# Optimization experiments

Measured on AMD Instinct MI355X. Metric: run time of the kernel, lower is better.

Reference implementation:

```python
import jax, jax.numpy as jnp
import numpy as np

N = 50000      # nodes
E = 800000     # edges
IN, HID, OUT, H = 128, 32, 128, 4
NEG_SLOPE = 0.2  # DGL GATConv default


def setup_inputs() -> dict:
    key = jax.random.key(0)
    ks = jax.random.split(key, 12)
    def w(k, shape, fan_in):
        return jax.random.normal(k, shape, dtype=jnp.float32) / np.sqrt(fan_in)
    return {
        "x": jax.random.normal(ks[0], (N, IN), dtype=jnp.float32),
        "src": jax.random.randint(ks[1], (E,), 0, N, dtype=jnp.int64),
        "dst": jax.random.randint(ks[2], (E,), 0, N, dtype=jnp.int64),
        # layer 0: GATConv(IN -> HID, H heads)
        "W0": w(ks[3], (IN, H * HID), IN),
        "attn_l0": w(ks[4], (H, HID), HID),
        "attn_r0": w(ks[5], (H, HID), HID),
        "bias0": jnp.zeros((H * HID,), dtype=jnp.float32),
        # layer 1: GATConv(H*HID -> OUT, 1 head)
        "W1": w(ks[6], (H * HID, OUT), H * HID),
        "attn_l1": w(ks[7], (1, OUT), OUT),
        "attn_r1": w(ks[8], (1, OUT), OUT),
        "bias1": jnp.zeros((OUT,), dtype=jnp.float32),
    }


def gat_conv(x, src, dst, W, attn_l, attn_r, bias, heads, feat_dim):
    """DGL GATConv: linear -> per-edge LeakyReLU attention -> edge softmax over
    destination neighborhoods -> weighted scatter-sum -> bias -> ELU."""
    n = x.shape[0]
    feat = (x @ W).reshape(n, heads, feat_dim)            # [N,H,F]
    el = jnp.einsum("nhf,hf->nh", feat, attn_l)           # [N,H]
    er = jnp.einsum("nhf,hf->nh", feat, attn_r)
    e = jax.nn.leaky_relu(el[src] + er[dst], NEG_SLOPE)    # [E,H]
    # segment softmax over incoming edges of each destination node
    e_max = jax.ops.segment_max(e, dst, num_segments=n)    # [N,H]
    exp_e = jnp.exp(e - e_max[dst])                        # [E,H]
    denom = jax.ops.segment_sum(exp_e, dst, num_segments=n)
    alpha = exp_e / denom[dst]                             # [E,H]
    msg = feat[src] * alpha[:, :, None]                    # [E,H,F]
    rst = jax.ops.segment_sum(msg, dst, num_segments=n)    # [N,H,F]
    rst = rst + bias.reshape(heads, feat_dim)
    return jax.nn.elu(rst)


def reference(x, src, dst, W0, attn_l0, attn_r0, bias0, W1, attn_l1, attn_r1, bias1):
    h = gat_conv(x, src, dst, W0, attn_l0, attn_r0, bias0, H, HID)   # [N,H,HID]
    h = h.reshape(h.shape[0], H * HID)                               # flatten(1)
    h = gat_conv(h, src, dst, W1, attn_l1, attn_r1, bias1, 1, OUT)   # [N,1,OUT]
    return h.mean(axis=1)                                            # [N,OUT]
```

## Files before the change

kernel.cpp:

```cpp
#include <hip/hip_runtime.h>

#define NEG_SLOPE 0.2f
#define NBMAX 256
#define BCAP 8192

typedef __attribute__((ext_vector_type(8))) short bf16x8;
typedef __attribute__((ext_vector_type(16))) float f32x16;

__device__ inline ushort bf16rne(float f) {
  uint u = __float_as_uint(f);
  u += 0x7fff + ((u >> 16) & 1);
  return (ushort)(u >> 16);
}
__device__ inline float bf2f(ushort h) { return __uint_as_float((uint)h << 16); }

#define XS(row, byte) ((byte) ^ (((row) & 15) << 4))

__global__ __launch_bounds__(256) void splitW2(const float* __restrict__ W0,
    const float* __restrict__ W1, ushort* __restrict__ W0h, ushort* __restrict__ W0l,
    ushort* __restrict__ W1h, ushort* __restrict__ W1l, int* __restrict__ bucketCursor) {
  if (blockIdx.x == 0 && threadIdx.x < NBMAX) bucketCursor[threadIdx.x] = 0;
  int g = blockIdx.x * 256 + threadIdx.x;
  const float* W = (g < 16384) ? W0 : W1;
  ushort* Wh = (g < 16384) ? W0h : W1h;
  ushort* Wl = (g < 16384) ? W0l : W1l;
  int i = g & 16383;
  int k = i >> 7, nn = i & 127;
  float w = W[i];
  ushort h = bf16rne(w);
  float lo = w - bf2f(h);
  Wh[nn * 128 + k] = h;
  Wl[nn * 128 + k] = bf16rne(lo);
}

__global__ __launch_bounds__(256) void prep_attn(const float* __restrict__ W0,
    const float* __restrict__ W1, const float* __restrict__ al0,
    const float* __restrict__ ar0, const float* __restrict__ al1,
    const float* __restrict__ ar1, float* __restrict__ wl0, float* __restrict__ wr0,
    float* __restrict__ wl1, float* __restrict__ wr1) {
  const int t = threadIdx.x;
  if (t < 128) {
    const int k = t;
#pragma unroll
    for (int h = 0; h < 4; ++h) {
      float sl = 0.f, sr = 0.f;
#pragma unroll
      for (int f = 0; f < 32; ++f) {
        float w = W0[k * 128 + h * 32 + f];
        sl += w * al0[h * 32 + f];
        sr += w * ar0[h * 32 + f];
      }
      wl0[h * 128 + k] = sl;
      wr0[h * 128 + k] = sr;
    }
  } else {
    const int k = t - 128;
    float sl = 0.f, sr = 0.f;
#pragma unroll
    for (int f = 0; f < 128; ++f) {
      float w = W1[k * 128 + f];
      sl += w * al1[f];
      sr += w * ar1[f];
    }
    wl1[k] = sl;
    wr1[k] = sr;
  }
}

__global__ __launch_bounds__(256) void gemm_mfma(const float* __restrict__ A,
    const ushort* __restrict__ Wh, const ushort* __restrict__ Wl,
    ushort* __restrict__ Cb, int n) {
  __shared__ __align__(16) ushort sAh[64 * 128];
  __shared__ __align__(16) ushort sAl[64 * 128];
  const int t = threadIdx.x;
  const int row0 = blockIdx.x * 64;
  const int col0 = blockIdx.y * 64;
  for (int i = t; i < 2048; i += 256) {
    int r = i >> 5, c4 = i & 31;
    int gr = row0 + r;
    float4 v = make_float4(0.f, 0.f, 0.f, 0.f);
    if (gr < n) v = ((const float4*)(A + (size_t)gr * 128))[c4];
    ushort4 h, l;
    h.x = bf16rne(v.x); l.x = bf16rne(v.x - bf2f(h.x));
    h.y = bf16rne(v.y); l.y = bf16rne(v.y - bf2f(h.y));
    h.z = bf16rne(v.z); l.z = bf16rne(v.z - bf2f(h.z));
    h.w = bf16rne(v.w); l.w = bf16rne(v.w - bf2f(h.w));
    int byte = XS(r, r * 256 + c4 * 8);
    *(ushort4*)((char*)sAh + byte) = h;
    *(ushort4*)((char*)sAl + byte) = l;
  }
  __syncthreads();
  const int wv = t >> 6, lane = t & 63;
  const int rbase = (wv >> 1) * 32;
  const int cbase = (wv & 1) * 32;
  const int lr = lane & 31;
  const int hi = lane >> 5;
  const int arow = rbase + lr;
  const int gcol = col0 + cbase + lr;
  const ushort* WhRow = Wh + (size_t)gcol * 128;
  const ushort* WlRow = Wl + (size_t)gcol * 128;
  f32x16 acc0 = {};
  f32x16 acc1 = {};
#pragma unroll
  for (int ks = 0; ks < 8; ++ks) {
    int k16 = ks * 16 + hi * 8;
    int kb = k16 * 2;
    bf16x8 ah = *(bf16x8*)((char*)sAh + XS(arow, arow * 256 + kb));
    bf16x8 al = *(bf16x8*)((char*)sAl + XS(arow, arow * 256 + kb));
    bf16x8 bh = *(const bf16x8*)(WhRow + k16);
    bf16x8 bl = *(const bf16x8*)(WlRow + k16);
    if (ks & 1) {
      acc1 = __builtin_amdgcn_mfma_f32_32x32x16_bf16(ah, bh, acc1, 0, 0, 0);
      acc1 = __builtin_amdgcn_mfma_f32_32x32x16_bf16(ah, bl, acc1, 0, 0, 0);
      acc1 = __builtin_amdgcn_mfma_f32_32x32x16_bf16(al, bh, acc1, 0, 0, 0);
    } else {
      acc0 = __builtin_amdgcn_mfma_f32_32x32x16_bf16(ah, bh, acc0, 0, 0, 0);
      acc0 = __builtin_amdgcn_mfma_f32_32x32x16_bf16(ah, bl, acc0, 0, 0, 0);
      acc0 = __builtin_amdgcn_mfma_f32_32x32x16_bf16(al, bh, acc0, 0, 0, 0);
    }
  }
#pragma unroll
  for (int r = 0; r < 16; ++r) {
    int grow = row0 + rbase + (r & 3) + 8 * (r >> 2) + 4 * hi;
    if (grow < n) Cb[(size_t)grow * 128 + gcol] = bf16rne(acc0[r] + acc1[r]);
  }
}

template <int HEADS>
__global__ __launch_bounds__(256) void node_attn(const float* __restrict__ A,
    const float* __restrict__ wl, const float* __restrict__ wr,
    float* __restrict__ el, float* __restrict__ er, int n) {
  __shared__ float swl[HEADS * 128];
  __shared__ float swr[HEADS * 128];
  for (int i = threadIdx.x; i < HEADS * 128; i += 256) {
    swl[i] = wl[i];
    swr[i] = wr[i];
  }
  __syncthreads();
  int i = blockIdx.x * 256 + threadIdx.x;
  if (i >= n) return;
  const float4* a4 = (const float4*)(A + (size_t)i * 128);
  float accl[HEADS], accr[HEADS];
#pragma unroll
  for (int h = 0; h < HEADS; ++h) { accl[h] = 0.f; accr[h] = 0.f; }
#pragma unroll 8
  for (int k4 = 0; k4 < 32; ++k4) {
    float4 v = a4[k4];
#pragma unroll
    for (int h = 0; h < HEADS; ++h) {
      float4 a = ((const float4*)(swl + h * 128))[k4];
      float4 b = ((const float4*)(swr + h * 128))[k4];
      accl[h] += v.x * a.x + v.y * a.y + v.z * a.z + v.w * a.w;
      accr[h] += v.x * b.x + v.y * b.y + v.z * b.z + v.w * b.w;
    }
  }
  if (HEADS == 4) {
    *(float4*)(el + (size_t)i * 4) = make_float4(accl[0], accl[1], accl[2], accl[3]);
    *(float4*)(er + (size_t)i * 4) = make_float4(accr[0], accr[1], accr[2], accr[3]);
  } else {
    el[i] = accl[0];
    er[i] = accr[0];
  }
}

__global__ __launch_bounds__(1024) void bucket_scatter(const int* __restrict__ src,
    const int* __restrict__ dst, int* __restrict__ bucketCursor,
    uint* __restrict__ bucketData, int E_) {
  __shared__ int h[NBMAX];
  __shared__ int bse[NBMAX];
  const int t = threadIdx.x;
  if (t < NBMAX) h[t] = 0;
  __syncthreads();
  const int base = blockIdx.x * 4096;
  int sv[4], dv[4], bk[4];
  bool ok[4];
#pragma unroll
  for (int k = 0; k < 4; ++k) {
    int i = base + k * 1024 + t;
    ok[k] = i < E_;
    if (ok[k]) {
      sv[k] = src[i];
      dv[k] = dst[i];
      bk[k] = dv[k] >> 8;
      atomicAdd(&h[bk[k]], 1);
    }
  }
  __syncthreads();
  if (t < NBMAX) {
    int c = h[t];
    bse[t] = c ? atomicAdd(&bucketCursor[t], c) : 0;
    h[t] = 0;
  }
  __syncthreads();
#pragma unroll
  for (int k = 0; k < 4; ++k) {
    if (ok[k]) {
      int r = atomicAdd(&h[bk[k]], 1);
      int pos = bse[bk[k]] + r;
      if (pos < BCAP)
        bucketData[(size_t)bk[k] * BCAP + pos] = (uint)sv[k] | ((uint)(dv[k] & 255) << 16);
    }
  }
}

__global__ __launch_bounds__(1024) void fine_csr(const uint* __restrict__ bucketData,
    const int* __restrict__ bucketCursor, int* __restrict__ rowbeg,
    int* __restrict__ rowend, uint* __restrict__ csr, int n) {
  __shared__ int fh[256];
  __shared__ int fx[256];
  const int b = blockIdx.x;
  const int t = threadIdx.x;
  const int beg = b * BCAP;
  int cnt = bucketCursor[b];
  if (cnt > BCAP) cnt = BCAP;
  if (t < 256) fh[t] = 0;
  __syncthreads();
  for (int i = t; i < cnt; i += 1024) atomicAdd(&fh[bucketData[beg + i] >> 16], 1);
  __syncthreads();
  if (t < 256) fx[t] = fh[t];
  __syncthreads();
  for (int off = 1; off < 256; off <<= 1) {
    int u = 0;
    if (t < 256 && t >= off) u = fx[t - off];
    __syncthreads();
    if (t < 256) fx[t] += u;
    __syncthreads();
  }
  if (t < 256) {
    int excl = fx[t] - fh[t];
    int node = b * 256 + t;
    if (node < n) {
      rowbeg[node] = beg + excl;
      rowend[node] = beg + fx[t];
    }
    fh[t] = excl;
  }
  __syncthreads();
  for (int i = t; i < cnt; i += 1024) {
    uint rec = bucketData[beg + i];
    int r = atomicAdd(&fh[rec >> 16], 1);
    csr[beg + r] = rec;
  }
}

__global__ __launch_bounds__(256) void aggregate4(const int* __restrict__ rowbeg,
    const int* __restrict__ rowend, const uint* __restrict__ csr,
    const ushort* __restrict__ featb, const float* __restrict__ el,
    const float* __restrict__ er, const float* __restrict__ bias,
    float* __restrict__ out, int n) {
  int node = blockIdx.x * 4 + (threadIdx.x >> 6);
  if (node >= n) return;
  const int lane = threadIdx.x & 63;
  const int f0 = lane * 2;
  const int h = lane >> 4;
  const float erh = er[(size_t)node * 4 + h];
  float a0 = 0.f, a1 = 0.f, d = 0.f;
  const int beg = rowbeg[node], end = rowend[node];
  int idx = beg;
  for (; idx + 7 < end; idx += 8) {
    int s0 = csr[idx + 0] & 0xffffu;
    int s1 = csr[idx + 1] & 0xffffu;
    int s2 = csr[idx + 2] & 0xffffu;
    int s3 = csr[idx + 3] & 0xffffu;
    int s4 = csr[idx + 4] & 0xffffu;
    int s5 = csr[idx + 5] & 0xffffu;
    int s6 = csr[idx + 6] & 0xffffu;
    int s7 = csr[idx + 7] & 0xffffu;
    float l0 = el[(size_t)s0 * 4 + h];
    float l1 = el[(size_t)s1 * 4 + h];
    float l2 = el[(size_t)s2 * 4 + h];
    float l3 = el[(size_t)s3 * 4 + h];
    float l4 = el[(size_t)s4 * 4 + h];
    float l5 = el[(size_t)s5 * 4 + h];
    float l6 = el[(size_t)s6 * 4 + h];
    float l7 = el[(size_t)s7 * 4 + h];
    uint v0 = *(const uint*)(featb + (size_t)s0 * 128 + f0);
    uint v1 = *(const uint*)(featb + (size_t)s1 * 128 + f0);
    uint v2 = *(const uint*)(featb + (size_t)s2 * 128 + f0);
    uint v3 = *(const uint*)(featb + (size_t)s3 * 128 + f0);
    uint v4 = *(const uint*)(featb + (size_t)s4 * 128 + f0);
    uint v5 = *(const uint*)(featb + (size_t)s5 * 128 + f0);
    uint v6 = *(const uint*)(featb + (size_t)s6 * 128 + f0);
    uint v7 = *(const uint*)(featb + (size_t)s7 * 128 + f0);
    float e0 = l0 + erh; e0 = e0 > 0.f ? e0 : NEG_SLOPE * e0; float w0 = __expf(e0);
    float e1 = l1 + erh; e1 = e1 > 0.f ? e1 : NEG_SLOPE * e1; float w1 = __expf(e1);
    float e2 = l2 + erh; e2 = e2 > 0.f ? e2 : NEG_SLOPE * e2; float w2 = __expf(e2);
    float e3 = l3 + erh; e3 = e3 > 0.f ? e3 : NEG_SLOPE * e3; float w3 = __expf(e3);
    float e4 = l4 + erh; e4 = e4 > 0.f ? e4 : NEG_SLOPE * e4; float w4 = __expf(e4);
    float e5 = l5 + erh; e5 = e5 > 0.f ? e5 : NEG_SLOPE * e5; float w5 = __expf(e5);
    float e6 = l6 + erh; e6 = e6 > 0.f ? e6 : NEG_SLOPE * e6; float w6 = __expf(e6);
    float e7 = l7 + erh; e7 = e7 > 0.f ? e7 : NEG_SLOPE * e7; float w7 = __expf(e7);
    a0 += __uint_as_float(v0 << 16) * w0; a1 += __uint_as_float(v0 & 0xffff0000u) * w0;
    a0 += __uint_as_float(v1 << 16) * w1; a1 += __uint_as_float(v1 & 0xffff0000u) * w1;
    a0 += __uint_as_float(v2 << 16) * w2; a1 += __uint_as_float(v2 & 0xffff0000u) * w2;
    a0 += __uint_as_float(v3 << 16) * w3; a1 += __uint_as_float(v3 & 0xffff0000u) * w3;
    a0 += __uint_as_float(v4 << 16) * w4; a1 += __uint_as_float(v4 & 0xffff0000u) * w4;
    a0 += __uint_as_float(v5 << 16) * w5; a1 += __uint_as_float(v5 & 0xffff0000u) * w5;
    a0 += __uint_as_float(v6 << 16) * w6; a1 += __uint_as_float(v6 & 0xffff0000u) * w6;
    a0 += __uint_as_float(v7 << 16) * w7; a1 += __uint_as_float(v7 & 0xffff0000u) * w7;
    d += w0 + w1 + w2 + w3 + w4 + w5 + w6 + w7;
  }
  for (; idx + 3 < end; idx += 4) {
    int s0 = csr[idx + 0] & 0xffffu;
    int s1 = csr[idx + 1] & 0xffffu;
    int s2 = csr[idx + 2] & 0xffffu;
    int s3 = csr[idx + 3] & 0xffffu;
    float l0 = el[(size_t)s0 * 4 + h];
    float l1 = el[(size_t)s1 * 4 + h];
    float l2 = el[(size_t)s2 * 4 + h];
    float l3 = el[(size_t)s3 * 4 + h];
    uint v0 = *(const uint*)(featb + (size_t)s0 * 128 + f0);
    uint v1 = *(const uint*)(featb + (size_t)s1 * 128 + f0);
    uint v2 = *(const uint*)(featb + (size_t)s2 * 128 + f0);
    uint v3 = *(const uint*)(featb + (size_t)s3 * 128 + f0);
    float e0 = l0 + erh; e0 = e0 > 0.f ? e0 : NEG_SLOPE * e0; float w0 = __expf(e0);
    float e1 = l1 + erh; e1 = e1 > 0.f ? e1 : NEG_SLOPE * e1; float w1 = __expf(e1);
    float e2 = l2 + erh; e2 = e2 > 0.f ? e2 : NEG_SLOPE * e2; float w2 = __expf(e2);
    float e3 = l3 + erh; e3 = e3 > 0.f ? e3 : NEG_SLOPE * e3; float w3 = __expf(e3);
    a0 += __uint_as_float(v0 << 16) * w0; a1 += __uint_as_float(v0 & 0xffff0000u) * w0;
    a0 += __uint_as_float(v1 << 16) * w1; a1 += __uint_as_float(v1 & 0xffff0000u) * w1;
    a0 += __uint_as_float(v2 << 16) * w2; a1 += __uint_as_float(v2 & 0xffff0000u) * w2;
    a0 += __uint_as_float(v3 << 16) * w3; a1 += __uint_as_float(v3 & 0xffff0000u) * w3;
    d += w0 + w1 + w2 + w3;
  }
  for (; idx < end; ++idx) {
    int s = csr[idx] & 0xffffu;
    float e = el[(size_t)s * 4 + h] + erh;
    e = e > 0.f ? e : NEG_SLOPE * e;
    float w = __expf(e);
    uint v = *(const uint*)(featb + (size_t)s * 128 + f0);
    a0 += __uint_as_float(v << 16) * w;
    a1 += __uint_as_float(v & 0xffff0000u) * w;
    d += w;
  }
  float inv = d > 0.f ? 1.f / d : 0.f;
  float v0 = a0 * inv + bias[f0];
  v0 = v0 > 0.f ? v0 : __expf(v0) - 1.f;
  float v1 = a1 * inv + bias[f0 + 1];
  v1 = v1 > 0.f ? v1 : __expf(v1) - 1.f;
  *(float2*)(out + (size_t)node * 128 + f0) = make_float2(v0, v1);
}

__global__ __launch_bounds__(256) void aggregate1(const int* __restrict__ rowbeg,
    const int* __restrict__ rowend, const uint* __restrict__ csr,
    const ushort* __restrict__ featb, const float* __restrict__ el,
    const float* __restrict__ er, const float* __restrict__ bias,
    float* __restrict__ out, int n) {
  int node = blockIdx.x * 4 + (threadIdx.x >> 6);
  if (node >= n) return;
  const int lane = threadIdx.x & 63;
  const int f0 = lane * 2;
  const float erv = er[node];
  float a0 = 0.f, a1 = 0.f, d = 0.f;
  const int beg = rowbeg[node], end = rowend[node];
  int idx = beg;
  for (; idx + 7 < end; idx += 8) {
    int s0 = csr[idx + 0] & 0xffffu;
    int s1 = csr[idx + 1] & 0xffffu;
    int s2 = csr[idx + 2] & 0xffffu;
    int s3 = csr[idx + 3] & 0xffffu;
    int s4 = csr[idx + 4] & 0xffffu;
    int s5 = csr[idx + 5] & 0xffffu;
    int s6 = csr[idx + 6] & 0xffffu;
    int s7 = csr[idx + 7] & 0xffffu;
    float l0 = el[s0];
    float l1 = el[s1];
    float l2 = el[s2];
    float l3 = el[s3];
    float l4 = el[s4];
    float l5 = el[s5];
    float l6 = el[s6];
    float l7 = el[s7];
    uint v0 = *(const uint*)(featb + (size_t)s0 * 128 + f0);
    uint v1 = *(const uint*)(featb + (size_t)s1 * 128 + f0);
    uint v2 = *(const uint*)(featb + (size_t)s2 * 128 + f0);
    uint v3 = *(const uint*)(featb + (size_t)s3 * 128 + f0);
    uint v4 = *(const uint*)(featb + (size_t)s4 * 128 + f0);
    uint v5 = *(const uint*)(featb + (size_t)s5 * 128 + f0);
    uint v6 = *(const uint*)(featb + (size_t)s6 * 128 + f0);
    uint v7 = *(const uint*)(featb + (size_t)s7 * 128 + f0);
    float e0 = l0 + erv; e0 = e0 > 0.f ? e0 : NEG_SLOPE * e0; float w0 = __expf(e0);
    float e1 = l1 + erv; e1 = e1 > 0.f ? e1 : NEG_SLOPE * e1; float w1 = __expf(e1);
    float e2 = l2 + erv; e2 = e2 > 0.f ? e2 : NEG_SLOPE * e2; float w2 = __expf(e2);
    float e3 = l3 + erv; e3 = e3 > 0.f ? e3 : NEG_SLOPE * e3; float w3 = __expf(e3);
    float e4 = l4 + erv; e4 = e4 > 0.f ? e4 : NEG_SLOPE * e4; float w4 = __expf(e4);
    float e5 = l5 + erv; e5 = e5 > 0.f ? e5 : NEG_SLOPE * e5; float w5 = __expf(e5);
    float e6 = l6 + erv; e6 = e6 > 0.f ? e6 : NEG_SLOPE * e6; float w6 = __expf(e6);
    float e7 = l7 + erv; e7 = e7 > 0.f ? e7 : NEG_SLOPE * e7; float w7 = __expf(e7);
    a0 += __uint_as_float(v0 << 16) * w0; a1 += __uint_as_float(v0 & 0xffff0000u) * w0;
    a0 += __uint_as_float(v1 << 16) * w1; a1 += __uint_as_float(v1 & 0xffff0000u) * w1;
    a0 += __uint_as_float(v2 << 16) * w2; a1 += __uint_as_float(v2 & 0xffff0000u) * w2;
    a0 += __uint_as_float(v3 << 16) * w3; a1 += __uint_as_float(v3 & 0xffff0000u) * w3;
    a0 += __uint_as_float(v4 << 16) * w4; a1 += __uint_as_float(v4 & 0xffff0000u) * w4;
    a0 += __uint_as_float(v5 << 16) * w5; a1 += __uint_as_float(v5 & 0xffff0000u) * w5;
    a0 += __uint_as_float(v6 << 16) * w6; a1 += __uint_as_float(v6 & 0xffff0000u) * w6;
    a0 += __uint_as_float(v7 << 16) * w7; a1 += __uint_as_float(v7 & 0xffff0000u) * w7;
    d += w0 + w1 + w2 + w3 + w4 + w5 + w6 + w7;
  }
  for (; idx + 3 < end; idx += 4) {
    int s0 = csr[idx + 0] & 0xffffu;
    int s1 = csr[idx + 1] & 0xffffu;
    int s2 = csr[idx + 2] & 0xffffu;
    int s3 = csr[idx + 3] & 0xffffu;
    float l0 = el[s0];
    float l1 = el[s1];
    float l2 = el[s2];
    float l3 = el[s3];
    uint v0 = *(const uint*)(featb + (size_t)s0 * 128 + f0);
    uint v1 = *(const uint*)(featb + (size_t)s1 * 128 + f0);
    uint v2 = *(const uint*)(featb + (size_t)s2 * 128 + f0);
    uint v3 = *(const uint*)(featb + (size_t)s3 * 128 + f0);
    float e0 = l0 + erv; e0 = e0 > 0.f ? e0 : NEG_SLOPE * e0; float w0 = __expf(e0);
    float e1 = l1 + erv; e1 = e1 > 0.f ? e1 : NEG_SLOPE * e1; float w1 = __expf(e1);
    float e2 = l2 + erv; e2 = e2 > 0.f ? e2 : NEG_SLOPE * e2; float w2 = __expf(e2);
    float e3 = l3 + erv; e3 = e3 > 0.f ? e3 : NEG_SLOPE * e3; float w3 = __expf(e3);
    a0 += __uint_as_float(v0 << 16) * w0; a1 += __uint_as_float(v0 & 0xffff0000u) * w0;
    a0 += __uint_as_float(v1 << 16) * w1; a1 += __uint_as_float(v1 & 0xffff0000u) * w1;
    a0 += __uint_as_float(v2 << 16) * w2; a1 += __uint_as_float(v2 & 0xffff0000u) * w2;
    a0 += __uint_as_float(v3 << 16) * w3; a1 += __uint_as_float(v3 & 0xffff0000u) * w3;
    d += w0 + w1 + w2 + w3;
  }
  for (; idx < end; ++idx) {
    int s = csr[idx] & 0xffffu;
    float e = el[s] + erv;
    e = e > 0.f ? e : NEG_SLOPE * e;
    float w = __expf(e);
    uint v = *(const uint*)(featb + (size_t)s * 128 + f0);
    a0 += __uint_as_float(v << 16) * w;
    a1 += __uint_as_float(v & 0xffff0000u) * w;
    d += w;
  }
  float inv = d > 0.f ? 1.f / d : 0.f;
  float v0 = a0 * inv + bias[f0];
  v0 = v0 > 0.f ? v0 : __expf(v0) - 1.f;
  float v1 = a1 * inv + bias[f0 + 1];
  v1 = v1 > 0.f ? v1 : __expf(v1) - 1.f;
  *(float2*)(out + (size_t)node * 128 + f0) = make_float2(v0, v1);
}

extern "C" void kernel_launch(void* const* d_in, const int* in_sizes, int n_in,
                              void* d_out, int out_size, void* d_ws, size_t ws_size,
                              hipStream_t stream) {
  const float* x   = (const float*)d_in[0];
  const int*   src = (const int*)d_in[1];
  const int*   dst = (const int*)d_in[2];
  const float* W0  = (const float*)d_in[3];
  const float* al0 = (const float*)d_in[4];
  const float* ar0 = (const float*)d_in[5];
  const float* b0  = (const float*)d_in[6];
  const float* W1  = (const float*)d_in[7];
  const float* al1 = (const float*)d_in[8];
  const float* ar1 = (const float*)d_in[9];
  const float* b1  = (const float*)d_in[10];
  float* out = (float*)d_out;
  const int n  = in_sizes[0] / 128;
  const int E_ = in_sizes[1];

  char* p = (char*)d_ws;
  auto alloc = [&](size_t bytes) {
    char* r = p;
    p += (bytes + 255) & ~(size_t)255;
    return r;
  };
  ushort* feat0b = (ushort*)alloc((size_t)n * 128 * 2);
  float*  h0     = (float*)alloc((size_t)n * 128 * 4);
  ushort* feat1b = (ushort*)alloc((size_t)n * 128 * 2);
  float* el0   = (float*)alloc((size_t)n * 4 * 4);
  float* er0   = (float*)alloc((size_t)n * 4 * 4);
  float* el1   = (float*)alloc((size_t)n * 4);
  float* er1   = (float*)alloc((size_t)n * 4);
  int* rowbeg  = (int*)alloc((size_t)n * 4);
  int* rowend  = (int*)alloc((size_t)n * 4);
  const int nbk = (n + 255) >> 8;
  uint* csr    = (uint*)alloc((size_t)nbk * BCAP * 4);
  uint* bucketData  = (uint*)alloc((size_t)nbk * BCAP * 4);
  int* bucketCursor = (int*)alloc(NBMAX * 4);
  ushort* W0h = (ushort*)alloc(128 * 128 * 2);
  ushort* W0l = (ushort*)alloc(128 * 128 * 2);
  ushort* W1h = (ushort*)alloc(128 * 128 * 2);
  ushort* W1l = (ushort*)alloc(128 * 128 * 2);
  float* wl0 = (float*)alloc(4 * 128 * 4);
  float* wr0 = (float*)alloc(4 * 128 * 4);
  float* wl1 = (float*)alloc(128 * 4);
  float* wr1 = (float*)alloc(128 * 4);

  const int gb  = (E_ + 4095) / 4096;
  const int nb256 = (n + 255) / 256;

  splitW2<<<128, 256, 0, stream>>>(W0, W1, W0h, W0l, W1h, W1l, bucketCursor);
  prep_attn<<<1, 256, 0, stream>>>(W0, W1, al0, ar0, al1, ar1, wl0, wr0, wl1, wr1);

  bucket_scatter<<<gb, 1024, 0, stream>>>(src, dst, bucketCursor, bucketData, E_);
  fine_csr<<<nbk, 1024, 0, stream>>>(bucketData, bucketCursor, rowbeg, rowend, csr, n);

  dim3 gg((n + 63) / 64, 2);

  node_attn<4><<<nb256, 256, 0, stream>>>(x, wl0, wr0, el0, er0, n);
  gemm_mfma<<<gg, 256, 0, stream>>>(x, W0h, W0l, feat0b, n);
  aggregate4<<<(n + 3) / 4, 256, 0, stream>>>(rowbeg, rowend, csr, feat0b, el0, er0, b0, h0, n);

  node_attn<1><<<nb256, 256, 0, stream>>>(h0, wl1, wr1, el1, er1, n);
  gemm_mfma<<<gg, 256, 0, stream>>>(h0, W1h, W1l, feat1b, n);
  aggregate1<<<(n + 3) / 4, 256, 0, stream>>>(rowbeg, rowend, csr, feat1b, el1, er1, b1, out, n);
}
```

Baseline: 171.1 us.

## Fuse attention-score computation into GEMM and merge prep_attn into splitW2

Removes the separate node_attn kernels. el/er are now computed inside gemm_mfma from the A tile already held in shared memory as a bf16 hi/lo split, which avoids a second full read of x and h0. prep_attn is folded into splitW2 as an extra block, removing another launch. The trade-offs are extra work in the y==0 GEMM blocks, possible LDS bank conflicts when four threads share a row, and a slight precision change from reconstructing A as hi+lo bf16.

```diff
diff --git a/kernel.cpp b/kernel.cpp
--- a/kernel.cpp
+++ b/kernel.cpp
@@ -18,9 +18,43 @@
 
 __global__ __launch_bounds__(256) void splitW2(const float* __restrict__ W0,
     const float* __restrict__ W1, ushort* __restrict__ W0h, ushort* __restrict__ W0l,
-    ushort* __restrict__ W1h, ushort* __restrict__ W1l, int* __restrict__ bucketCursor) {
-  if (blockIdx.x == 0 && threadIdx.x < NBMAX) bucketCursor[threadIdx.x] = 0;
-  int g = blockIdx.x * 256 + threadIdx.x;
+    ushort* __restrict__ W1h, ushort* __restrict__ W1l, int* __restrict__ bucketCursor,
+    const float* __restrict__ al0, const float* __restrict__ ar0,
+    const float* __restrict__ al1, const float* __restrict__ ar1,
+    float* __restrict__ wl0, float* __restrict__ wr0,
+    float* __restrict__ wl1, float* __restrict__ wr1) {
+  const int t = threadIdx.x;
+  if (blockIdx.x == 128) {
+    if (t < 128) {
+      const int k = t;
+#pragma unroll
+      for (int h = 0; h < 4; ++h) {
+        float sl = 0.f, sr = 0.f;
+#pragma unroll
+        for (int f = 0; f < 32; ++f) {
+          float w = W0[k * 128 + h * 32 + f];
+          sl += w * al0[h * 32 + f];
+          sr += w * ar0[h * 32 + f];
+        }
+        wl0[h * 128 + k] = sl;
+        wr0[h * 128 + k] = sr;
+      }
+    } else {
+      const int k = t - 128;
+      float sl = 0.f, sr = 0.f;
+#pragma unroll
+      for (int f = 0; f < 128; ++f) {
+        float w = W1[k * 128 + f];
+        sl += w * al1[f];
+        sr += w * ar1[f];
+      }
+      wl1[k] = sl;
+      wr1[k] = sr;
+    }
+    return;
+  }
+  if (blockIdx.x == 0 && t < NBMAX) bucketCursor[t] = 0;
+  int g = blockIdx.x * 256 + t;
   const float* W = (g < 16384) ? W0 : W1;
   ushort* Wh = (g < 16384) ? W0h : W1h;
   ushort* Wl = (g < 16384) ? W0l : W1l;
@@ -33,43 +67,11 @@
   Wl[nn * 128 + k] = bf16rne(lo);
 }
 
-__global__ __launch_bounds__(256) void prep_attn(const float* __restrict__ W0,
-    const float* __restrict__ W1, const float* __restrict__ al0,
-    const float* __restrict__ ar0, const float* __restrict__ al1,
-    const float* __restrict__ ar1, float* __restrict__ wl0, float* __restrict__ wr0,
-    float* __restrict__ wl1, float* __restrict__ wr1) {
-  const int t = threadIdx.x;
-  if (t < 128) {
-    const int k = t;
-#pragma unroll
-    for (int h = 0; h < 4; ++h) {
-      float sl = 0.f, sr = 0.f;
-#pragma unroll
-      for (int f = 0; f < 32; ++f) {
-        float w = W0[k * 128 + h * 32 + f];
-        sl += w * al0[h * 32 + f];
-        sr += w * ar0[h * 32 + f];
-      }
-      wl0[h * 128 + k] = sl;
-      wr0[h * 128 + k] = sr;
-    }
-  } else {
-    const int k = t - 128;
-    float sl = 0.f, sr = 0.f;
-#pragma unroll
-    for (int f = 0; f < 128; ++f) {
-      float w = W1[k * 128 + f];
-      sl += w * al1[f];
-      sr += w * ar1[f];
-    }
-    wl1[k] = sl;
-    wr1[k] = sr;
-  }
-}
-
 __global__ __launch_bounds__(256) void gemm_mfma(const float* __restrict__ A,
     const ushort* __restrict__ Wh, const ushort* __restrict__ Wl,
-    ushort* __restrict__ Cb, int n) {
+    ushort* __restrict__ Cb, const float* __restrict__ wl,
+    const float* __restrict__ wr, float* __restrict__ el, float* __restrict__ er,
+    int heads, int n) {
   __shared__ __align__(16) ushort sAh[64 * 128];
   __shared__ __align__(16) ushort sAl[64 * 128];
   const int t = threadIdx.x;
@@ -124,42 +126,51 @@
     int grow = row0 + rbase + (r & 3) + 8 * (r >> 2) + 4 * hi;
     if (grow < n) Cb[(size_t)grow * 128 + gcol] = bf16rne(acc0[r] + acc1[r]);
   }
-}
-
-template <int HEADS>
-__global__ __launch_bounds__(256) void node_attn(const float* __restrict__ A,
-    const float* __restrict__ wl, const float* __restrict__ wr,
-    float* __restrict__ el, float* __restrict__ er, int n) {
-  __shared__ float swl[HEADS * 128];
-  __shared__ float swr[HEADS * 128];
-  for (int i = threadIdx.x; i < HEADS * 128; i += 256) {
-    swl[i] = wl[i];
-    swr[i] = wr[i];
-  }
-  __syncthreads();
-  int i = blockIdx.x * 256 + threadIdx.x;
-  if (i >= n) return;
-  const float4* a4 = (const float4*)(A + (size_t)i * 128);
-  float accl[HEADS], accr[HEADS];
-#pragma unroll
-  for (int h = 0; h < HEADS; ++h) { accl[h] = 0.f; accr[h] = 0.f; }
-#pragma unroll 8
-  for (int k4 = 0; k4 < 32; ++k4) {
-    float4 v = a4[k4];
-#pragma unroll
-    for (int h = 0; h < HEADS; ++h) {
-      float4 a = ((const float4*)(swl + h * 128))[k4];
-      float4 b = ((const float4*)(swr + h * 128))[k4];
-      accl[h] += v.x * a.x + v.y * a.y + v.z * a.z + v.w * a.w;
-      accr[h] += v.x * b.x + v.y * b.y + v.z * b.z + v.w * b.w;
+  if (blockIdx.y == 0) {
+    if (heads == 4) {
+      const int row = t >> 2;
+      const int h = t & 3;
+      const float* wlh = wl + h * 128;
+      const float* wrh = wr + h * 128;
+      float sl = 0.f, sr = 0.f;
+#pragma unroll
+      for (int c = 0; c < 16; ++c) {
+        int kb = c * 16;
+        bf16x8 hh = *(bf16x8*)((char*)sAh + XS(row, row * 256 + kb));
+        bf16x8 ll = *(bf16x8*)((char*)sAl + XS(row, row * 256 + kb));
+#pragma unroll
+        for (int j = 0; j < 8; ++j) {
+          float xv = bf2f((ushort)hh[j]) + bf2f((ushort)ll[j]);
+          sl += xv * wlh[c * 8 + j];
+          sr += xv * wrh[c * 8 + j];
+        }
+      }
+      int grow = row0 + row;
+      if (grow < n) {
+        el[(size_t)grow * 4 + h] = sl;
+        er[(size_t)grow * 4 + h] = sr;
+      }
+    } else if (t < 64) {
+      const int row = t;
+      float sl = 0.f, sr = 0.f;
+#pragma unroll
+      for (int c = 0; c < 16; ++c) {
+        int kb = c * 16;
+        bf16x8 hh = *(bf16x8*)((char*)sAh + XS(row, row * 256 + kb));
+        bf16x8 ll = *(bf16x8*)((char*)sAl + XS(row, row * 256 + kb));
+#pragma unroll
+        for (int j = 0; j < 8; ++j) {
+          float xv = bf2f((ushort)hh[j]) + bf2f((ushort)ll[j]);
+          sl += xv * wl[c * 8 + j];
+          sr += xv * wr[c * 8 + j];
+        }
+      }
+      int grow = row0 + row;
+      if (grow < n) {
+        el[grow] = sl;
+        er[grow] = sr;
+      }
     }
-  }
-  if (HEADS == 4) {
-    *(float4*)(el + (size_t)i * 4) = make_float4(accl[0], accl[1], accl[2], accl[3]);
-    *(float4*)(er + (size_t)i * 4) = make_float4(accr[0], accr[1], accr[2], accr[3]);
-  } else {
-    el[i] = accl[0];
-    er[i] = accr[0];
   }
 }
 
@@ -484,22 +495,19 @@
   float* wl1 = (float*)alloc(128 * 4);
   float* wr1 = (float*)alloc(128 * 4);
 
-  const int gb  = (E_ + 4095) / 4096;
-  const int nb256 = (n + 255) / 256;
-
-  splitW2<<<128, 256, 0, stream>>>(W0, W1, W0h, W0l, W1h, W1l, bucketCursor);
-  prep_attn<<<1, 256, 0, stream>>>(W0, W1, al0, ar0, al1, ar1, wl0, wr0, wl1, wr1);
+  const int gb = (E_ + 4095) / 4096;
+
+  splitW2<<<129, 256, 0, stream>>>(W0, W1, W0h, W0l, W1h, W1l, bucketCursor,
+                                   al0, ar0, al1, ar1, wl0, wr0, wl1, wr1);
 
   bucket_scatter<<<gb, 1024, 0, stream>>>(src, dst, bucketCursor, bucketData, E_);
   fine_csr<<<nbk, 1024, 0, stream>>>(bucketData, bucketCursor, rowbeg, rowend, csr, n);
 
   dim3 gg((n + 63) / 64, 2);
 
-  node_attn<4><<<nb256, 256, 0, stream>>>(x, wl0, wr0, el0, er0, n);
-  gemm_mfma<<<gg, 256, 0, stream>>>(x, W0h, W0l, feat0b, n);
+  gemm_mfma<<<gg, 256, 0, stream>>>(x, W0h, W0l, feat0b, wl0, wr0, el0, er0, 4, n);
   aggregate4<<<(n + 3) / 4, 256, 0, stream>>>(rowbeg, rowend, csr, feat0b, el0, er0, b0, h0, n);
 
-  node_attn<1><<<nb256, 256, 0, stream>>>(h0, wl1, wr1, el1, er1, n);
-  gemm_mfma<<<gg, 256, 0, stream>>>(h0, W1h, W1l, feat1b, n);
+  gemm_mfma<<<gg, 256, 0, stream>>>(h0, W1h, W1l, feat1b, wl1, wr1, el1, er1, 1, n);
   aggregate1<<<(n + 3) / 4, 256, 0, stream>>>(rowbeg, rowend, csr, feat1b, el1, er1, b1, out, n);
 }
```

After: 213.5 us. 24.7% more time.
